# Kernel tuning notes

Measured on AMD Instinct MI355X. Metric: run time of the kernel, lower is better.

## Reference

```python
import jax, jax.numpy as jnp
import numpy as np

BITS = 4
GROUP = 128
IN_F = 4096
OUT_F = 4096
MASK = (1 << BITS) - 1  # 15
# non-uniform 4-bit codebook from QuantLinear (AF / AbnormalFloat style)
CODE = jnp.array([-6, -4, -3, -2, -1.5, -1, -0.5, -0.0,
                   0.0, 0.5, 1, 1.5, 2, 3, 4, 6], dtype=jnp.float32)


def setup_inputs() -> dict:
    key = jax.random.key(0)
    k1, k2, k3, k4, k5 = jax.random.split(key, 5)
    x = jax.random.normal(k1, (4, 2048, IN_F), dtype=jnp.float32)
    qweight = jax.random.randint(k2, (IN_F // 32 * BITS, OUT_F), 0, 2147483647, dtype=jnp.int32)
    n_groups = IN_F // GROUP
    scales = jax.random.uniform(k3, (n_groups, OUT_F), dtype=jnp.float32, minval=0.01, maxval=0.1)
    scales2 = jax.random.uniform(k4, (n_groups, OUT_F), dtype=jnp.float32, minval=0.01, maxval=0.1)
    bias = jax.random.normal(k5, (OUT_F,), dtype=jnp.float32)
    return {"x": x, "qweight": qweight, "scales": scales, "scales2": scales2, "bias": bias}


def dequantize(qweight, scales, scales2):
    # unpack: (rows, OUT) -> (rows, 8, OUT) nibbles; matches torch right_shift + & maxq
    wf = jnp.arange(0, 32, BITS, dtype=jnp.int32)          # (8,)
    q = (qweight[:, None, :] >> wf[None, :, None]) & MASK  # (IN/8, 8, OUT) ints in [0,15]
    q = q.reshape(IN_F // GROUP, GROUP, OUT_F)             # group-major layout
    w = CODE[q]                                            # codebook lookup
    # two-scale: positive codes use scales, negative codes use scales2 (per group, per out-col)
    w = jnp.where(w >= 0, w * scales[:, None, :], w * scales2[:, None, :])
    return w.reshape(IN_F, OUT_F)


def reference(x, qweight, scales, scales2, bias):
    W = dequantize(qweight, scales, scales2)        # (IN_F, OUT_F)
    out = jnp.einsum('bsi,io->bso', x, W) + bias    # grouped-dequant matmul + bias
    return out
```

## Files before the change

kernel.cpp:

```cpp
#include <hip/hip_runtime.h>
#include <hip/hip_bf16.h>
#include <stdint.h>

#define M_ROWS 8192
#define K_DIM  4096
#define N_DIM  4096

using bf16 = __hip_bfloat16;
typedef __attribute__((ext_vector_type(4))) float f32x4;
typedef __attribute__((ext_vector_type(8))) short s16x8;

__device__ __forceinline__ void gll16(const bf16* g, bf16* l) {
  __builtin_amdgcn_global_load_lds(
      (const __attribute__((address_space(1))) void*)g,
      (__attribute__((address_space(3))) void*)l, 16, 0, 0);
}

__global__ __launch_bounds__(256) void prep_k(
    const int* __restrict__ qw, const float* __restrict__ s1,
    const float* __restrict__ s2, const float* __restrict__ x,
    bf16* __restrict__ Bp, bf16* __restrict__ Ap)
{
  const int bid = blockIdx.x;
  if (bid < 2048) {
    const int t = bid * 256 + threadIdx.x;
    const int o = t & 4095;
    const int q = t >> 12;
    const int r0 = q << 2;
    const int g = r0 >> 4;
    const int nt = o >> 8, col = o & 255;
    const int sw = (col >> 1) & 3;
    const float a = s1[g * 4096 + o] * 0.5f;
    const float b = s2[g * 4096 + o] * 0.5f;
    const uint64_t lo = 0x00FFFEFDFCFAF8F4ull;
    const uint64_t hi = 0x0C08060403020100ull;
    bf16* dst = Bp + (((size_t)(nt * 128 + q)) << 13) + col * 32;
    #pragma unroll
    for (int j = 0; j < 4; ++j) {
      const uint32_t wbits = (uint32_t)qw[(size_t)(r0 + j) * 4096 + o];
      union { bf16 h[8]; s16x8 v; } u;
      #pragma unroll
      for (int i = 0; i < 8; ++i) {
        const int qc = (wbits >> (4 * i)) & 15;
        const uint64_t pk = (qc & 8) ? hi : lo;
        const int c2 = (int)(int8_t)(uint8_t)(pk >> ((qc & 7) * 8));
        const float sc = (qc & 8) ? a : b;
        u.h[i] = __float2bfloat16((float)c2 * sc);
      }
      *(s16x8*)(dst + ((j ^ sw) << 3)) = u.v;
    }
  } else {
    const int t = (bid - 2048) * 256 + threadIdx.x;
    const int k8 = t & 511;
    const int kt = k8 >> 2;
    const int s_lin = k8 & 3;
    const int m  = t >> 9;
    const int tm = m >> 7, row = m & 127;
    const float* s = x + (size_t)m * 4096 + k8 * 8;
    f32x4 v0 = *(const f32x4*)s;
    f32x4 v1 = *(const f32x4*)(s + 4);
    union { bf16 h[8]; s16x8 v; } u;
    #pragma unroll
    for (int j = 0; j < 4; ++j) {
      u.h[j]     = __float2bfloat16(v0[j]);
      u.h[4 + j] = __float2bfloat16(v1[j]);
    }
    const int ss = s_lin ^ ((row >> 1) & 3);
    bf16* dst = Ap + (((size_t)(tm * 128 + kt)) << 12) + row * 32 + ss * 8;
    *(s16x8*)dst = u.v;
  }
}

#define BAR()                                                         \
    asm volatile("s_barrier" ::: "memory");                           \
    __builtin_amdgcn_sched_barrier(0)

#define PH_SYNC()                                                     \
    asm volatile("s_barrier" ::: "memory");                           \
    asm volatile("s_waitcnt lgkmcnt(0)" ::: "memory");                \
    __builtin_amdgcn_sched_barrier(0)

#define VMW(N)                                                        \
    asm volatile("s_waitcnt vmcnt(" #N ")" ::: "memory");             \
    __builtin_amdgcn_sched_barrier(0)

#define KT9(BUF, KTN, PRE, VM)                                        \
  {                                                                   \
    const bf16* L_ = &lds[BUF][0];                                    \
    _Pragma("unroll")                                                 \
    for (int m = 0; m < 4; ++m) af[m] = *(const s16x8*)(L_ + aoff + m * 512); \
    _Pragma("unroll")                                                 \
    for (int n = 0; n < 4; ++n) bb[n] = *(const s16x8*)(L_ + boff + n * 512); \
    if (PRE) stage((KTN), ((BUF) + 2) % 3);                           \
    PH_SYNC();                                                        \
    __builtin_amdgcn_s_setprio(1);                                    \
    _Pragma("unroll")                                                 \
    for (int m = 0; m < 4; ++m) {                                     \
      _Pragma("unroll")                                               \
      for (int n = 0; n < 4; ++n)                                     \
        acc[m][n] = __builtin_amdgcn_mfma_f32_16x16x32_bf16(          \
            af[m], bb[n], acc[m][n], 0, 0, 0);                        \
    }                                                                 \
    __builtin_amdgcn_s_setprio(0);                                    \
    VMW(VM);                                                          \
    BAR();                                                            \
  }

__global__ __launch_bounds__(512, 4) void gemm9_k(
    const bf16* __restrict__ Ap, const bf16* __restrict__ Bp,
    const float* __restrict__ bias, float* __restrict__ out)
{
  __shared__ bf16 lds[3][12288];

  const int id  = blockIdx.x;
  const int xcd = id & 7, lid = id >> 3;
  const int tn  = lid >> 3;
  const int tm  = xcd * 8 + (lid & 7);
  const int tid = (int)threadIdx.x;
  const int lane = tid & 63;
  const int w   = tid >> 6;
  const int wr  = w >> 2;
  const int wc  = w & 3;
  const int lr  = lane & 15;
  const int lg  = lane >> 4;
  const int sl  = (lg ^ ((lr >> 1) & 3)) << 3;
  const int aoff = (wr * 64 + lr) * 32 + sl;
  const int boff = 4096 + (wc * 64 + lr) * 32 + sl;

  const bf16* Abase = Ap + ((size_t)tm << 19);
  const bf16* Bbase = Bp + ((size_t)tn << 20);

  f32x4 acc[4][4];
  #pragma unroll
  for (int m = 0; m < 4; ++m)
    #pragma unroll
    for (int n = 0; n < 4; ++n) acc[m][n] = (f32x4){0.f, 0.f, 0.f, 0.f};

  auto stage = [&](int kt, int buf) {
    gll16(Abase + ((size_t)kt << 12) + tid * 8, &lds[buf][tid * 8]);
    const bf16* bs = Bbase + ((size_t)kt << 13) + tid * 8;
    gll16(bs,        &lds[buf][4096 + tid * 8]);
    gll16(bs + 4096, &lds[buf][8192 + tid * 8]);
  };

  s16x8 af[4], bb[4];

  stage(0, 0);
  stage(1, 1);
  VMW(3);
  BAR();

  #pragma unroll 1
  for (int t3 = 0; t3 < 42; ++t3) {
    KT9(0, 3 * t3 + 2, 1, 3);
    KT9(1, 3 * t3 + 3, 1, 3);
    KT9(2, 3 * t3 + 4, 1, 3);
  }
  KT9(0, 0, 0, 0);
  KT9(1, 0, 0, 0);

  const int orow0 = tm * 128 + wr * 64 + lg * 4;
  const int ocol0 = tn * 256 + wc * 64 + lr;
  float bv[4];
  #pragma unroll
  for (int n = 0; n < 4; ++n) bv[n] = bias[ocol0 + n * 16];
  #pragma unroll
  for (int m = 0; m < 4; ++m) {
    #pragma unroll
    for (int r = 0; r < 4; ++r) {
      float* op = out + (size_t)(orow0 + m * 16 + r) * N_DIM + ocol0;
      #pragma unroll
      for (int n = 0; n < 4; ++n) op[n * 16] = acc[m][n][r] + bv[n];
    }
  }
}

__global__ __launch_bounds__(256) void dequant_f(
    const int* __restrict__ qw, const float* __restrict__ s1,
    const float* __restrict__ s2, bf16* __restrict__ Bp)
{
  const int t = blockIdx.x * 256 + threadIdx.x;
  const int o = t & 4095;
  const int r = t >> 12;
  const int g = r >> 4;
  const int kt = r >> 2;
  const int kk0 = (r & 3) * 8;
  const uint32_t wbits = (uint32_t)qw[(size_t)r * 4096 + o];
  const float a = s1[g * 4096 + o] * 0.5f;
  const float b = s2[g * 4096 + o] * 0.5f;
  const uint64_t lo = 0x00FFFEFDFCFAF8F4ull;
  const uint64_t hi = 0x0C08060403020100ull;
  union { bf16 h[8]; s16x8 v; } u;
  #pragma unroll
  for (int j = 0; j < 8; ++j) {
    const int q = (wbits >> (4 * j)) & 15;
    const uint64_t pk = (q & 8) ? hi : lo;
    const int c2 = (int)(int8_t)(uint8_t)(pk >> ((q & 7) * 8));
    const float s = (q & 8) ? a : b;
    u.h[j] = __float2bfloat16((float)c2 * s);
  }
  const int nt = o >> 7, col = o & 127;
  bf16* dst = Bp + (((size_t)(nt * 128 + kt) * 128 + col) * 32 + kk0);
  *(s16x8*)dst = u.v;
}

__global__ __launch_bounds__(256) void gemmf_k(
    const float* __restrict__ x, const bf16* __restrict__ Bp,
    const float* __restrict__ bias, float* __restrict__ out)
{
  __shared__ bf16 As[2][4096];
  __shared__ bf16 Bs[2][4096];

  const int id  = blockIdx.x;
  const int swz = (id & 7) * 256 + (id >> 3);
  const int tm  = swz >> 5;
  const int tn  = swz & 31;
  const int tid = threadIdx.x;
  const int lane = tid & 63;
  const int w   = tid >> 6;
  const int wr  = (w >> 1) * 64;
  const int wc  = (w & 1) * 64;
  const int lr  = lane & 15;
  const int lg  = lane >> 4;

  f32x4 acc[4][4];
  #pragma unroll
  for (int m = 0; m < 4; ++m)
    #pragma unroll
    for (int n = 0; n < 4; ++n) acc[m][n] = (f32x4){0.f, 0.f, 0.f, 0.f};

  const bf16* bsrc = Bp + ((size_t)tn << 19);
  const float* asrc_f = x + ((size_t)(tm * 128 + (tid >> 1)) << 12) + (tid & 1) * 16;
  float areg[16];

  auto stageB = [&](int kt, int buf) {
    const bf16* bs = bsrc + ((size_t)kt << 12);
    gll16(bs + tid * 8,        &Bs[buf][tid * 8]);
    gll16(bs + 2048 + tid * 8, &Bs[buf][2048 + tid * 8]);
  };
  auto loadA = [&](int kt) {
    const float* s = asrc_f + ((size_t)kt << 5);
    #pragma unroll
    for (int i = 0; i < 4; ++i)
      *(f32x4*)(areg + i * 4) = *(const f32x4*)(s + i * 4);
  };
  auto writeA = [&](int buf) {
    union { bf16 h[16]; s16x8 v[2]; } u;
    #pragma unroll
    for (int i = 0; i < 16; ++i) u.h[i] = __float2bfloat16(areg[i]);
    bf16* d = &As[buf][(tid >> 1) * 32 + (tid & 1) * 16];
    *(s16x8*)d = u.v[0];
    *(s16x8*)(d + 8) = u.v[1];
  };
  auto compute = [&](int buf) {
    s16x8 af[4], bv[4];
    #pragma unroll
    for (int m = 0; m < 4; ++m)
      af[m] = *(const s16x8*)(&As[buf][(wr + m * 16 + lr) * 32 + lg * 8]);
    #pragma unroll
    for (int n = 0; n < 4; ++n)
      bv[n] = *(const s16x8*)(&Bs[buf][(wc + n * 16 + lr) * 32 + lg * 8]);
    #pragma unroll
    for (int m = 0; m < 4; ++m)
      #pragma unroll
      for (int n = 0; n < 4; ++n)
        acc[m][n] = __builtin_amdgcn_mfma_f32_16x16x32_bf16(af[m], bv[n],
                                                            acc[m][n], 0, 0, 0);
  };

  stageB(0, 0);
  loadA(0);
  writeA(0);
  __syncthreads();

  #pragma unroll 2
  for (int kt = 0; kt < 128; ++kt) {
    const int buf = kt & 1;
    if (kt + 1 < 128) {
      stageB(kt + 1, buf ^ 1);
      loadA(kt + 1);
    }
    compute(buf);
    if (kt + 1 < 128) writeA(buf ^ 1);
    __syncthreads();
  }

  const int orow0 = tm * 128 + wr + lg * 4;
  const int ocol0 = tn * 128 + wc + lr;
  float bvv[4];
  #pragma unroll
  for (int n = 0; n < 4; ++n) bvv[n] = bias[ocol0 + n * 16];
  #pragma unroll
  for (int m = 0; m < 4; ++m) {
    #pragma unroll
    for (int r = 0; r < 4; ++r) {
      float* op = out + (size_t)(orow0 + m * 16 + r) * N_DIM + ocol0;
      #pragma unroll
      for (int n = 0; n < 4; ++n)
        op[n * 16] = acc[m][n][r] + bvv[n];
    }
  }
}

extern "C" void kernel_launch(void* const* d_in, const int* in_sizes, int n_in,
                              void* d_out, int out_size, void* d_ws, size_t ws_size,
                              hipStream_t stream) {
  const float* x    = (const float*)d_in[0];
  const int*   qw   = (const int*)d_in[1];
  const float* s1   = (const float*)d_in[2];
  const float* s2   = (const float*)d_in[3];
  const float* bias = (const float*)d_in[4];
  float* out = (float*)d_out;

  const size_t BP_BYTES = (size_t)K_DIM * N_DIM * 2;
  const size_t XB_BYTES = (size_t)M_ROWS * K_DIM * 2;
  bf16* Bp = (bf16*)d_ws;

  if (ws_size >= BP_BYTES + XB_BYTES) {
    bf16* Ap = (bf16*)((char*)d_ws + BP_BYTES);
    prep_k<<<dim3(18432), dim3(256), 0, stream>>>(qw, s1, s2, x, Bp, Ap);
    gemm9_k<<<dim3(1024), dim3(512), 0, stream>>>(Ap, Bp, bias, out);
  } else {
    dequant_f<<<dim3(8192), dim3(256), 0, stream>>>(qw, s1, s2, Bp);
    gemmf_k<<<dim3(2048), dim3(256), 0, stream>>>(x, Bp, bias, out);
  }
}
```

Before: 271.0 us.

## Switch GEMM inner loop to 32x32x16 MFMA and drop phase barrier

Replaces the 4x4 grid of 16x16x32 bf16 MFMAs per wave with a 2x2 grid of 32x32x16 MFMAs over two k-halves, changing the LDS fragment addressing (swizzled offsets per half-wave) and the output store mapping. It also removes the s_barrier before the compute phase and keeps only the lgkmcnt wait. The larger MFMA shape is meant to reduce LDS read traffic per FLOP and raise matrix-core efficiency. It risks a different register footprint and store pattern, and dropping the barrier relies on the existing end-of-step barrier to keep buffers safe.

```diff
diff --git a/kernel.cpp b/kernel.cpp
--- a/kernel.cpp
+++ b/kernel.cpp
@@ -7,8 +7,9 @@
 #define N_DIM  4096
 
 using bf16 = __hip_bfloat16;
-typedef __attribute__((ext_vector_type(4))) float f32x4;
-typedef __attribute__((ext_vector_type(8))) short s16x8;
+typedef __attribute__((ext_vector_type(4)))  float f32x4;
+typedef __attribute__((ext_vector_type(16))) float f32x16;
+typedef __attribute__((ext_vector_type(8)))  short s16x8;
 
 __device__ __forceinline__ void gll16(const bf16* g, bf16* l) {
   __builtin_amdgcn_global_load_lds(
@@ -75,8 +76,7 @@
     asm volatile("s_barrier" ::: "memory");                           \
     __builtin_amdgcn_sched_barrier(0)
 
-#define PH_SYNC()                                                     \
-    asm volatile("s_barrier" ::: "memory");                           \
+#define LGKM0()                                                       \
     asm volatile("s_waitcnt lgkmcnt(0)" ::: "memory");                \
     __builtin_amdgcn_sched_barrier(0)
 
@@ -87,20 +87,28 @@
 #define KT9(BUF, KTN, PRE, VM)                                        \
   {                                                                   \
     const bf16* L_ = &lds[BUF][0];                                    \
+    s16x8 afr[2][2], bbr[2][2];                                       \
     _Pragma("unroll")                                                 \
-    for (int m = 0; m < 4; ++m) af[m] = *(const s16x8*)(L_ + aoff + m * 512); \
+    for (int m = 0; m < 2; ++m)                                       \
+      _Pragma("unroll")                                               \
+      for (int kk = 0; kk < 2; ++kk)                                  \
+        afr[m][kk] = *(const s16x8*)(L_ + abase + m * 1024 + soff[kk]); \
     _Pragma("unroll")                                                 \
-    for (int n = 0; n < 4; ++n) bb[n] = *(const s16x8*)(L_ + boff + n * 512); \
+    for (int n = 0; n < 2; ++n)                                       \
+      _Pragma("unroll")                                               \
+      for (int kk = 0; kk < 2; ++kk)                                  \
+        bbr[n][kk] = *(const s16x8*)(L_ + bbase + n * 1024 + soff[kk]); \
     if (PRE) stage((KTN), ((BUF) + 2) % 3);                           \
-    PH_SYNC();                                                        \
+    LGKM0();                                                          \
     __builtin_amdgcn_s_setprio(1);                                    \
     _Pragma("unroll")                                                 \
-    for (int m = 0; m < 4; ++m) {                                     \
+    for (int kk = 0; kk < 2; ++kk)                                    \
       _Pragma("unroll")                                               \
-      for (int n = 0; n < 4; ++n)                                     \
-        acc[m][n] = __builtin_amdgcn_mfma_f32_16x16x32_bf16(          \
-            af[m], bb[n], acc[m][n], 0, 0, 0);                        \
-    }                                                                 \
+      for (int m = 0; m < 2; ++m)                                     \
+        _Pragma("unroll")                                             \
+        for (int n = 0; n < 2; ++n)                                   \
+          acc[m][n] = __builtin_amdgcn_mfma_f32_32x32x16_bf16(        \
+              afr[m][kk], bbr[n][kk], acc[m][n], 0, 0, 0);            \
     __builtin_amdgcn_s_setprio(0);                                    \
     VMW(VM);                                                          \
     BAR();                                                            \
@@ -118,23 +126,28 @@
   const int tm  = xcd * 8 + (lid & 7);
   const int tid = (int)threadIdx.x;
   const int lane = tid & 63;
-  const int w   = tid >> 6;
-  const int wr  = w >> 2;
-  const int wc  = w & 3;
-  const int lr  = lane & 15;
-  const int lg  = lane >> 4;
-  const int sl  = (lg ^ ((lr >> 1) & 3)) << 3;
-  const int aoff = (wr * 64 + lr) * 32 + sl;
-  const int boff = 4096 + (wc * 64 + lr) * 32 + sl;
+  const int w    = tid >> 6;
+  const int wr   = w >> 2;
+  const int wc   = w & 3;
+  const int lr32 = lane & 31;
+  const int hi   = lane >> 5;
+  const int sx   = (lr32 >> 1) & 3;
+  int soff[2];
+  soff[0] = ((0 * 2 + hi) ^ sx) * 8;
+  soff[1] = ((1 * 2 + hi) ^ sx) * 8;
+  const int abase = (wr * 64 + lr32) * 32;
+  const int bbase = 4096 + (wc * 64 + lr32) * 32;
 
   const bf16* Abase = Ap + ((size_t)tm << 19);
   const bf16* Bbase = Bp + ((size_t)tn << 20);
 
-  f32x4 acc[4][4];
-  #pragma unroll
-  for (int m = 0; m < 4; ++m)
-    #pragma unroll
-    for (int n = 0; n < 4; ++n) acc[m][n] = (f32x4){0.f, 0.f, 0.f, 0.f};
+  f32x16 acc[2][2];
+  #pragma unroll
+  for (int m = 0; m < 2; ++m)
+    #pragma unroll
+    for (int n = 0; n < 2; ++n)
+      #pragma unroll
+      for (int r = 0; r < 16; ++r) acc[m][n][r] = 0.f;
 
   auto stage = [&](int kt, int buf) {
     gll16(Abase + ((size_t)kt << 12) + tid * 8, &lds[buf][tid * 8]);
@@ -143,8 +156,6 @@
     gll16(bs + 4096, &lds[buf][8192 + tid * 8]);
   };
 
-  s16x8 af[4], bb[4];
-
   stage(0, 0);
   stage(1, 1);
   VMW(3);
@@ -159,18 +170,19 @@
   KT9(0, 0, 0, 0);
   KT9(1, 0, 0, 0);
 
-  const int orow0 = tm * 128 + wr * 64 + lg * 4;
-  const int ocol0 = tn * 256 + wc * 64 + lr;
-  float bv[4];
-  #pragma unroll
-  for (int n = 0; n < 4; ++n) bv[n] = bias[ocol0 + n * 16];
-  #pragma unroll
-  for (int m = 0; m < 4; ++m) {
-    #pragma unroll
-    for (int r = 0; r < 4; ++r) {
-      float* op = out + (size_t)(orow0 + m * 16 + r) * N_DIM + ocol0;
-      #pragma unroll
-      for (int n = 0; n < 4; ++n) op[n * 16] = acc[m][n][r] + bv[n];
+  const int orow0 = tm * 128 + wr * 64 + hi * 4;
+  const int ocol0 = tn * 256 + wc * 64 + lr32;
+  #pragma unroll
+  for (int m = 0; m < 2; ++m) {
+    #pragma unroll
+    for (int n = 0; n < 2; ++n) {
+      const int col = ocol0 + n * 32;
+      const float bv = bias[col];
+      #pragma unroll
+      for (int r = 0; r < 16; ++r) {
+        const int row = orow0 + m * 32 + (r & 3) + 8 * (r >> 2);
+        out[(size_t)row * N_DIM + col] = acc[m][n][r] + bv;
+      }
     }
   }
 }
```

Measured after the change: 314.4 us. 1.16x slower.
